# Kernel tuning notes

Hardware: AMD Instinct MI355X
Metric: run time of the kernel (lower is better)

Reference implementation:

```python
import jax, jax.numpy as jnp
import numpy as np

BN_EPS = 1e-5


def _conv1x1(x, w, b=None):
    # x: [B,C,H,W], w: [O,C] (1x1 conv kernel squeezed)
    y = jnp.einsum('bchw,oc->bohw', x, w)
    if b is not None:
        y = y + b[None, :, None, None]
    return y


def _maxpool2(x):
    B, C, H, W = x.shape
    return x.reshape(B, C, H // 2, 2, W // 2, 2).max(axis=(3, 5))


def setup_inputs() -> dict:
    key = jax.random.key(0)
    ks = jax.random.split(key, 14)
    B, C, H, W = 8, 128, 64, 64
    IC = C // 2  # inter_channels
    s = 0.05
    f32 = jnp.float32
    return {
        'x': jax.random.normal(ks[0], (B, C, H, W), f32),
        'w1': jax.random.normal(ks[1], (IC, C), f32) * s,
        'b1': jax.random.normal(ks[2], (IC,), f32) * s,
        'w3': jax.random.normal(ks[3], (IC, C), f32) * s,
        'b3': jax.random.normal(ks[4], (IC,), f32) * s,
        'w4': jax.random.normal(ks[5], (IC, C), f32) * s,
        'b4': jax.random.normal(ks[6], (IC,), f32) * s,
        'w5': jax.random.normal(ks[7], (2 * IC,), f32) * s,  # conv5_pr, no bias
        'w2': jax.random.normal(ks[8], (C, IC), f32) * s,  # zero-init in torch; randomized for a non-trivial baseline
        'b2': jax.random.normal(ks[9], (C,), f32) * s,
        'bn_gamma': 1.0 + jax.random.normal(ks[10], (C,), f32) * 0.1,
        'bn_beta': jax.random.normal(ks[11], (C,), f32) * 0.1,
        'bn_mean': jax.random.normal(ks[12], (C,), f32) * 0.1,
        'bn_var': jax.random.uniform(ks[13], (C,), f32, 0.5, 1.5),
    }


def reference(x, w1, b1, w3, b3, w4, b4, w5, w2, b2, bn_gamma, bn_beta, bn_mean, bn_var):
    B, C, H, W = x.shape
    IC = C // 2
    N = H * W            # query positions
    # value branch: conv1 -> maxpool -> [B, M, IC]
    xg = _maxpool2(_conv1x1(x, w1, b1)).reshape(B, IC, -1)  # [B, IC, M]
    M = xg.shape[-1]
    xg = xg.transpose(0, 2, 1)  # [B, M, IC]
    # affinity: relu(w5 . cat(xt_i, xp_j)) is separable -> avoid [B,2IC,N,M] blowup
    xt = _conv1x1(x, w3, b3).reshape(B, IC, N)              # [B, IC, N]
    xp = _maxpool2(_conv1x1(x, w4, b4)).reshape(B, IC, M)   # [B, IC, M]
    wt, wp = w5[:IC], w5[IC:]
    logits = jnp.einsum('c,bcn->bn', wt, xt)[:, :, None] + \
             jnp.einsum('c,bcm->bm', wp, xp)[:, None, :]    # [B, N, M]
    feats = jax.nn.relu(logits) / M
    # aggregate
    y = jnp.einsum('bnm,bmi->bni', feats, xg)               # [B, N, IC]
    y = y.transpose(0, 2, 1).reshape(B, IC, H, W)
    # conv2 + batchnorm (eval mode, running stats)
    y = _conv1x1(y, w2, b2)
    inv = jax.lax.rsqrt(bn_var + BN_EPS)
    y = (y - bn_mean[None, :, None, None]) * (bn_gamma * inv)[None, :, None, None] + bn_beta[None, :, None, None]
    return y + x
```

## Files before the change

### kernel.cpp

```cpp
#include <hip/hip_runtime.h>

typedef unsigned int u32;
typedef unsigned short u16;

#define Cn 128
#define ICn 64
#define Nn 4096
#define Mn 1024

typedef __attribute__((ext_vector_type(8))) short s8v;
typedef __attribute__((ext_vector_type(4))) float f4v;

__device__ __forceinline__ float bf2f(u16 u){ union{u32 i; float f;} v; v.i = ((u32)u) << 16; return v.f; }
__device__ __forceinline__ u16 f2bf(float f){ union{float f; u32 i;} v; v.f = f; u32 r = v.i + 0x7fffu + ((v.i >> 16) & 1u); return (u16)(r >> 16); }
__device__ __forceinline__ u32 pk2(float lo, float hi){ return (u32)f2bf(lo) | ((u32)f2bf(hi) << 16); }

__global__ __launch_bounds__(256) void k_conv(
    const float* __restrict__ x,
    const float* __restrict__ w1, const float* __restrict__ b1,
    const float* __restrict__ w3, const float* __restrict__ b3,
    const float* __restrict__ w4, const float* __restrict__ b4,
    const float* __restrict__ w5, const float* __restrict__ w2,
    float* __restrict__ t_o, float* __restrict__ p_o, float* __restrict__ g_o)
{
    const int tile = blockIdx.x;
    const int r  = tile >> 1;
    const int wb = tile & 1;
    const int b  = blockIdx.y;
    const int tid = threadIdx.x;

    __shared__ __align__(16) u16 smem[32768];
    u16* xsT = smem;
    u16* w1t = smem + 8704;
    u16* w4t = smem + 17408;
    float* ph = (float*)&smem[26112];
    u16* w2t = smem + 8704;
    u16* xgr = smem + 17920;
    float* u3s = (float*)&smem[30464];

    #pragma unroll
    for (int it = 0; it < 4; ++it) {
        int f = tid + 256 * it;
        int cp = f >> 4, rem = f & 15;
        int rl = rem >> 3, wq = rem & 7;
        const float* src = x + ((size_t)(b * Cn + 2 * cp)) * Nn + (2 * r + rl) * 64 + 32 * wb + 4 * wq;
        float4 v0 = *(const float4*)src;
        float4 v1 = *(const float4*)(src + Nn);
        int lp0 = rl * 32 + 4 * wq;
        int cS = (2 * cp) ^ (wq << 3);
        *(u32*)&xsT[(lp0 + 0) * 136 + cS] = pk2(v0.x, v1.x);
        *(u32*)&xsT[(lp0 + 1) * 136 + cS] = pk2(v0.y, v1.y);
        *(u32*)&xsT[(lp0 + 2) * 136 + cS] = pk2(v0.z, v1.z);
        *(u32*)&xsT[(lp0 + 3) * 136 + cS] = pk2(v0.w, v1.w);
    }
    #pragma unroll
    for (int it = 0; it < 4; ++it) {
        int f = tid + 256 * it;
        int ic = f >> 4, cq = f & 15;
        const float4* s1 = (const float4*)&w1[f * 8];
        const float4* s4 = (const float4*)&w4[f * 8];
        float4 a0 = s1[0], a1v = s1[1];
        float4 d0 = s4[0], d1v = s4[1];
        uint4 A, D;
        A.x = pk2(a0.x, a0.y); A.y = pk2(a0.z, a0.w); A.z = pk2(a1v.x, a1v.y); A.w = pk2(a1v.z, a1v.w);
        D.x = pk2(d0.x, d0.y); D.y = pk2(d0.z, d0.w); D.z = pk2(d1v.x, d1v.y); D.w = pk2(d1v.z, d1v.w);
        *(uint4*)&w1t[ic * 136 + 8 * cq] = A;
        *(uint4*)&w4t[ic * 136 + 8 * cq] = D;
    }
    if (tid < 128) {
        float s0 = 0.f, s1 = 0.f;
        #pragma unroll 8
        for (int ic = 0; ic < 64; ic += 2) {
            s0 += w5[ic]     * w3[ic * Cn + tid];
            s1 += w5[ic + 1] * w3[(ic + 1) * Cn + tid];
        }
        u3s[tid] = s0 + s1;
    } else if (tid == 128) {
        float s = 0.f;
        #pragma unroll 16
        for (int ic = 0; ic < 64; ++ic) s += w5[ic] * b3[ic];
        u3s[128] = s;
    }
    __syncthreads();

    const int lane = tid & 63;
    const int wv   = tid >> 6;
    const int col  = lane & 15;
    const int quad = lane >> 4;

    f4v acc1[4] = {}, acc4[4] = {};
    const u16* xrow = &xsT[(16 * wv + col) * 136];
    const int xsw = (((16 * wv + col) >> 2) & 7) << 3;
    #pragma unroll
    for (int kb = 0; kb < 4; ++kb) {
        s8v bx = *(const s8v*)&xrow[(kb * 32 + quad * 8) ^ xsw];
        #pragma unroll
        for (int icb = 0; icb < 4; ++icb) {
            s8v a1 = *(const s8v*)&w1t[(icb * 16 + col) * 136 + kb * 32 + quad * 8];
            s8v a4 = *(const s8v*)&w4t[(icb * 16 + col) * 136 + kb * 32 + quad * 8];
            acc1[icb] = __builtin_amdgcn_mfma_f32_16x16x32_bf16(a1, bx, acc1[icb], 0, 0, 0);
            acc4[icb] = __builtin_amdgcn_mfma_f32_16x16x32_bf16(a4, bx, acc4[icb], 0, 0, 0);
        }
    }
    __syncthreads();

    const int lp = 16 * wv + col;
    const int rl = lp >> 5, wl = lp & 31, pw = wl >> 1;
    const bool wr = (wl & 1) == 0;
    #pragma unroll
    for (int icb = 0; icb < 4; ++icb)
        #pragma unroll
        for (int reg = 0; reg < 4; ++reg) {
            float v = acc1[icb][reg];
            float vm = fmaxf(v, __shfl_xor(v, 1, 64));
            if (wr) ph[(rl * 16 + pw) * 68 + icb * 16 + quad * 4 + reg] = vm;
        }
    __syncthreads();

    #pragma unroll
    for (int it = 0; it < 4; ++it) {
        int e = tid + 256 * it;
        int pwq = e >> 6, ic = e & 63;
        float v = fmaxf(ph[pwq * 68 + ic], ph[(16 + pwq) * 68 + ic]) + b1[ic];
        xgr[pwq * 72 + ic] = f2bf(v);
    }
    {
        int px = tid >> 2, part = tid & 3;
        const int tsw = ((px >> 2) & 7) << 3;
        const u16* xr = &xsT[px * 136];
        float s = 0.f;
        #pragma unroll
        for (int cq = 0; cq < 4; ++cq) {
            int u = part * 32 + cq * 8;
            s8v xv = *(const s8v*)&xr[u ^ tsw];
            #pragma unroll
            for (int j = 0; j < 8; ++j) s += u3s[u + j] * bf2f((u16)xv[j]);
        }
        s += __shfl_xor(s, 1, 64);
        s += __shfl_xor(s, 2, 64);
        if (part == 0)
            t_o[(size_t)b * Nn + (2 * r + (px >> 5)) * 64 + 32 * wb + (px & 31)] = s + u3s[128];
    }
    __syncthreads();

    #pragma unroll
    for (int it = 0; it < 4; ++it) {
        int f = tid + 256 * it;
        int co = f >> 3, iq = f & 7;
        const float4* s2 = (const float4*)&w2[f * 8];
        float4 a0 = s2[0], a1v = s2[1];
        uint4 V;
        V.x = pk2(a0.x, a0.y); V.y = pk2(a0.z, a0.w); V.z = pk2(a1v.x, a1v.y); V.w = pk2(a1v.z, a1v.w);
        *(uint4*)&w2t[co * 72 + 8 * iq] = V;
    }
    #pragma unroll
    for (int icb = 0; icb < 4; ++icb)
        #pragma unroll
        for (int reg = 0; reg < 4; ++reg) {
            float v = acc4[icb][reg];
            float vm = fmaxf(v, __shfl_xor(v, 1, 64));
            if (wr) ph[(rl * 16 + pw) * 68 + icb * 16 + quad * 4 + reg] = vm;
        }
    __syncthreads();

    #pragma unroll
    for (int cob2 = 0; cob2 < 2; ++cob2) {
        int cob = 2 * wv + cob2;
        f4v gacc = {};
        #pragma unroll
        for (int kb = 0; kb < 2; ++kb) {
            s8v a  = *(const s8v*)&xgr[col * 72 + kb * 32 + quad * 8];
            s8v bb = *(const s8v*)&w2t[(cob * 16 + col) * 72 + kb * 32 + quad * 8];
            gacc = __builtin_amdgcn_mfma_f32_16x16x32_bf16(a, bb, gacc, 0, 0, 0);
        }
        #pragma unroll
        for (int reg = 0; reg < 4; ++reg) {
            int pwr = quad * 4 + reg;
            int m = r * 32 + wb * 16 + pwr;
            g_o[((size_t)b * Mn + m) * 128 + cob * 16 + col] = gacc[reg];
        }
    }

    if (tid < 16) {
        float s = 0.f;
        #pragma unroll 8
        for (int ic = 0; ic < 64; ++ic) {
            float pv = fmaxf(ph[tid * 68 + ic], ph[(16 + tid) * 68 + ic]) + b4[ic];
            s += w5[64 + ic] * pv;
        }
        p_o[(size_t)b * Mn + r * 32 + wb * 16 + tid] = s;
    }
}

__global__ __launch_bounds__(512) void k_rank(
    const float* __restrict__ p, float* __restrict__ ps, int* __restrict__ perm)
{
    const int seg = blockIdx.x;
    const int b   = blockIdx.y;
    const int tid = threadIdx.x;
    __shared__ float pls[1024];
    #pragma unroll
    for (int it = 0; it < 2; ++it) pls[tid + 512 * it] = p[b * 1024 + tid + 512 * it];
    __syncthreads();
    const int m = seg * 32 + (tid >> 4);
    const int sub = tid & 15;
    const float key = pls[m];
    int rank = 0;
    #pragma unroll 8
    for (int jj = 0; jj < 64; ++jj) {
        int j = sub + jj * 16;
        float v = pls[j];
        rank += (v < key || (v == key && j < m)) ? 1 : 0;
    }
    rank += __shfl_xor(rank, 1, 64);
    rank += __shfl_xor(rank, 2, 64);
    rank += __shfl_xor(rank, 4, 64);
    rank += __shfl_xor(rank, 8, 64);
    if (sub == 0) {
        ps[b * 1024 + rank]   = key;
        perm[b * 1024 + rank] = m;
    }
}

__global__ __launch_bounds__(512) void k_scanA(
    const float* __restrict__ g, const float* __restrict__ ps, const int* __restrict__ perm,
    float2* __restrict__ csab)
{
    const int seg = blockIdx.x;
    const int b = blockIdx.y;
    const int tid = threadIdx.x;
    const int co = tid & 127, jh = tid >> 7;
    __shared__ float redA[4][128], redB[4][128];
    __shared__ float pl[32];
    __shared__ int   pml[32];
    if (tid < 32) { pl[tid] = ps[b * 1024 + seg * 32 + tid]; pml[tid] = perm[b * 1024 + seg * 32 + tid]; }
    __syncthreads();
    float sA = 0.f, sB = 0.f;
    #pragma unroll
    for (int jj = jh * 8; jj < jh * 8 + 8; ++jj) {
        float gv = g[((size_t)b * Mn + pml[jj]) * 128 + co];
        sA += gv; sB += pl[jj] * gv;
    }
    redA[jh][co] = sA; redB[jh][co] = sB;
    __syncthreads();
    if (tid < 128) {
        float2 v;
        v.x = (redA[0][tid] + redA[1][tid]) + (redA[2][tid] + redA[3][tid]);
        v.y = (redB[0][tid] + redB[1][tid]) + (redB[2][tid] + redB[3][tid]);
        csab[(b * 32 + seg) * 128 + tid] = v;
    }
}

__global__ __launch_bounds__(512) void k_scanC(
    const float* __restrict__ g, const float* __restrict__ ps, const int* __restrict__ perm,
    const float2* __restrict__ csab, float2* __restrict__ SAB)
{
    const int seg = blockIdx.x;
    const int b = blockIdx.y;
    const int tid = threadIdx.x;
    __shared__ float gs[32 * 128];
    __shared__ float pl[32];
    __shared__ int   pml[32];
    if (tid < 32) { pl[tid] = ps[b * 1024 + seg * 32 + tid]; pml[tid] = perm[b * 1024 + seg * 32 + tid]; }
    __syncthreads();
    #pragma unroll
    for (int it = 0; it < 8; ++it) {
        int f = tid + 512 * it;
        int jj = f >> 7, co = f & 127;
        gs[jj * 128 + co] = g[((size_t)b * Mn + pml[jj]) * 128 + co];
    }
    __syncthreads();

    if (tid < 128) {
        const int co = tid;
        float rA = 0.f, rB = 0.f;
        #pragma unroll 4
        for (int s2 = seg + 1; s2 < 32; ++s2) {
            float2 v = csab[(b * 32 + s2) * 128 + co];
            rA += v.x; rB += v.y;
        }
        if (seg == 31) SAB[((size_t)b * 1025 + 1024) * 128 + co] = make_float2(0.f, 0.f);
        #pragma unroll
        for (int jj = 31; jj >= 0; --jj) {
            float gv = gs[jj * 128 + co];
            rA += gv;
            rB += pl[jj] * gv;
            SAB[((size_t)b * 1025 + seg * 32 + jj) * 128 + co] = make_float2(rA, rB);
        }
    }
}

__global__ __launch_bounds__(512) void k_final(
    const float* __restrict__ x, const float* __restrict__ t,
    const float* __restrict__ ps, const float2* __restrict__ SAB,
    const float* __restrict__ b2, const float* __restrict__ gamma, const float* __restrict__ beta,
    const float* __restrict__ mean, const float* __restrict__ var,
    float* __restrict__ out)
{
    const int nt = blockIdx.x;
    const int b = blockIdx.y;
    const int tid = threadIdx.x;
    const int n0 = nt * 128;
    __shared__ float psl[1024];
    __shared__ float tl[128];
    __shared__ int   kl[128];
    __shared__ float sc[128], bs[128];
    __shared__ float sa_s[32][129], sb_s[32][129];

    #pragma unroll
    for (int it = 0; it < 2; ++it) psl[tid + 512 * it] = ps[b * 1024 + tid + 512 * it];
    __syncthreads();
    if (tid < 128) {
        float tv = t[(size_t)b * Nn + n0 + tid];
        tl[tid] = tv;
        float key = -tv;
        int lo = 0, hi = 1024;
        while (lo < hi) { int mid = (lo + hi) >> 1; if (psl[mid] > key) hi = mid; else lo = mid + 1; }
        kl[tid] = lo;
    } else if (tid < 256) {
        int co = tid - 128;
        float s = gamma[co] * rsqrtf(var[co] + 1e-5f);
        sc[co] = s * (1.0f / 1024.0f);
        bs[co] = (b2[co] - mean[co]) * s + beta[co];
    }
    __syncthreads();

    float2 pf[8], pf2[8];
    {
        #pragma unroll
        for (int i2 = 0; i2 < 8; ++i2) {
            int f = tid + 512 * i2;
            int rowl = f >> 7, co = f & 127;
            pf[i2] = SAB[((size_t)b * 1025 + kl[rowl]) * 128 + co];
        }
    }
    for (int sub = 0; sub < 4; ++sub) {
        #pragma unroll
        for (int i2 = 0; i2 < 8; ++i2) {
            int f = tid + 512 * i2;
            int rowl = f >> 7, co = f & 127;
            sa_s[rowl][co] = pf[i2].x;
            sb_s[rowl][co] = pf[i2].y;
        }
        if (sub < 3) {
            #pragma unroll
            for (int i2 = 0; i2 < 8; ++i2) {
                int f = tid + 512 * i2;
                int rowl = f >> 7, co = f & 127;
                pf2[i2] = SAB[((size_t)b * 1025 + kl[(sub + 1) * 32 + rowl]) * 128 + co];
            }
        }
        __syncthreads();
        #pragma unroll
        for (int it = 0; it < 2; ++it) {
            int f = tid + 512 * it;
            int co = f >> 3, nn0 = (f & 7) * 4;
            size_t gidx = ((size_t)b * Cn + co) * Nn + n0 + sub * 32 + nn0;
            float4 xv = *(const float4*)&x[gidx];
            float scv = sc[co], bsv = bs[co];
            float4 o;
            float v0 = tl[sub*32+nn0+0] * sa_s[nn0+0][co] + sb_s[nn0+0][co];
            float v1 = tl[sub*32+nn0+1] * sa_s[nn0+1][co] + sb_s[nn0+1][co];
            float v2 = tl[sub*32+nn0+2] * sa_s[nn0+2][co] + sb_s[nn0+2][co];
            float v3 = tl[sub*32+nn0+3] * sa_s[nn0+3][co] + sb_s[nn0+3][co];
            o.x = v0 * scv + bsv + xv.x;
            o.y = v1 * scv + bsv + xv.y;
            o.z = v2 * scv + bsv + xv.z;
            o.w = v3 * scv + bsv + xv.w;
            *(float4*)&out[gidx] = o;
        }
        __syncthreads();
        #pragma unroll
        for (int i2 = 0; i2 < 8; ++i2) pf[i2] = pf2[i2];
    }
}

extern "C" void kernel_launch(void* const* d_in, const int* in_sizes, int n_in,
                              void* d_out, int out_size, void* d_ws, size_t ws_size,
                              hipStream_t stream)
{
    const float* x  = (const float*)d_in[0];
    const float* w1 = (const float*)d_in[1];
    const float* b1 = (const float*)d_in[2];
    const float* w3 = (const float*)d_in[3];
    const float* b3 = (const float*)d_in[4];
    const float* w4 = (const float*)d_in[5];
    const float* b4 = (const float*)d_in[6];
    const float* w5 = (const float*)d_in[7];
    const float* w2 = (const float*)d_in[8];
    const float* b2 = (const float*)d_in[9];
    const float* gm = (const float*)d_in[10];
    const float* bt = (const float*)d_in[11];
    const float* mn = (const float*)d_in[12];
    const float* vr = (const float*)d_in[13];
    float* out = (float*)d_out;

    float* ws = (float*)d_ws;
    const size_t FTOT = 3823872;
    if (ws_size < FTOT * sizeof(float)) return;

    float*  t_w  = ws;
    float*  p_w  = ws + 32768;
    float*  ps_w = ws + 40960;
    int*    pm_w = (int*)(ws + 49152);
    float*  g_w  = ws + 581632;
    float2* csab = (float2*)(ws + 1630208);
    float2* SAB  = (float2*)(ws + 1695744);

    k_conv <<<dim3(64, 8), 256, 0, stream>>>(x, w1, b1, w3, b3, w4, b4, w5, w2,
                                             t_w, p_w, g_w);
    k_rank <<<dim3(32, 8), 512, 0, stream>>>(p_w, ps_w, pm_w);
    k_scanA<<<dim3(32, 8), 512, 0, stream>>>(g_w, ps_w, pm_w, csab);
    k_scanC<<<dim3(32, 8), 512, 0, stream>>>(g_w, ps_w, pm_w, csab, SAB);
    k_final<<<dim3(32, 8), 512, 0, stream>>>(x, t_w, ps_w, SAB, b2, gm, bt, mn, vr, out);
}
```

Baseline: 122.5 us.

## Stage conv weights in K-halves, add occupancy bound, and parallelize suffix scan

k_conv now loads the w1/w4 weights into shared memory in two K-halves, each with a 72-element row stride, and adds a launch-bounds min-blocks hint of 3. The shared buffer is re-laid out with byte offsets to fit the new staging plan. k_scanC now uses all 512 threads instead of 128: each group of 128 threads computes a local sum over 8 of the 32 rows, the groups exchange those partial sums through shared memory, and each group then runs its own segment of the reverse scan. The intent is higher occupancy and more parallel work in the scan, at the cost of extra barriers and a second weight-load phase in the conv kernel.

```diff
diff --git a/kernel.cpp b/kernel.cpp
--- a/kernel.cpp
+++ b/kernel.cpp
@@ -15,7 +15,7 @@
 __device__ __forceinline__ u16 f2bf(float f){ union{float f; u32 i;} v; v.f = f; u32 r = v.i + 0x7fffu + ((v.i >> 16) & 1u); return (u16)(r >> 16); }
 __device__ __forceinline__ u32 pk2(float lo, float hi){ return (u32)f2bf(lo) | ((u32)f2bf(hi) << 16); }
 
-__global__ __launch_bounds__(256) void k_conv(
+__global__ __launch_bounds__(256, 3) void k_conv(
     const float* __restrict__ x,
     const float* __restrict__ w1, const float* __restrict__ b1,
     const float* __restrict__ w3, const float* __restrict__ b3,
@@ -29,14 +29,14 @@
     const int b  = blockIdx.y;
     const int tid = threadIdx.x;
 
-    __shared__ __align__(16) u16 smem[32768];
-    u16* xsT = smem;
-    u16* w1t = smem + 8704;
-    u16* w4t = smem + 17408;
-    float* ph = (float*)&smem[26112];
-    u16* w2t = smem + 8704;
-    u16* xgr = smem + 17920;
-    float* u3s = (float*)&smem[30464];
+    __shared__ __align__(16) char smem[47368];
+    u16* xsT = (u16*)smem;
+    u16* wt1 = (u16*)(smem + 17408);
+    u16* wt4 = (u16*)(smem + 26624);
+    u16* w2t = (u16*)(smem + 17408);
+    float* ph = (float*)(smem + 35840);
+    u16* xgr = (u16*)(smem + 44544);
+    float* u3s = (float*)(smem + 46848);
 
     #pragma unroll
     for (int it = 0; it < 4; ++it) {
@@ -54,18 +54,18 @@
         *(u32*)&xsT[(lp0 + 3) * 136 + cS] = pk2(v0.w, v1.w);
     }
     #pragma unroll
-    for (int it = 0; it < 4; ++it) {
+    for (int it = 0; it < 2; ++it) {
         int f = tid + 256 * it;
-        int ic = f >> 4, cq = f & 15;
-        const float4* s1 = (const float4*)&w1[f * 8];
-        const float4* s4 = (const float4*)&w4[f * 8];
-        float4 a0 = s1[0], a1v = s1[1];
-        float4 d0 = s4[0], d1v = s4[1];
+        int ic = f >> 3, cq = f & 7;
+        const float* s1 = &w1[ic * Cn + 8 * cq];
+        const float* s4 = &w4[ic * Cn + 8 * cq];
+        float4 a0 = *(const float4*)s1, a1v = *(const float4*)(s1 + 4);
+        float4 d0 = *(const float4*)s4, d1v = *(const float4*)(s4 + 4);
         uint4 A, D;
         A.x = pk2(a0.x, a0.y); A.y = pk2(a0.z, a0.w); A.z = pk2(a1v.x, a1v.y); A.w = pk2(a1v.z, a1v.w);
         D.x = pk2(d0.x, d0.y); D.y = pk2(d0.z, d0.w); D.z = pk2(d1v.x, d1v.y); D.w = pk2(d1v.z, d1v.w);
-        *(uint4*)&w1t[ic * 136 + 8 * cq] = A;
-        *(uint4*)&w4t[ic * 136 + 8 * cq] = D;
+        *(uint4*)&wt1[ic * 72 + 8 * cq] = A;
+        *(uint4*)&wt4[ic * 72 + 8 * cq] = D;
     }
     if (tid < 128) {
         float s0 = 0.f, s1 = 0.f;
@@ -91,15 +91,38 @@
     f4v acc1[4] = {}, acc4[4] = {};
     const u16* xrow = &xsT[(16 * wv + col) * 136];
     const int xsw = (((16 * wv + col) >> 2) & 7) << 3;
-    #pragma unroll
-    for (int kb = 0; kb < 4; ++kb) {
-        s8v bx = *(const s8v*)&xrow[(kb * 32 + quad * 8) ^ xsw];
-        #pragma unroll
-        for (int icb = 0; icb < 4; ++icb) {
-            s8v a1 = *(const s8v*)&w1t[(icb * 16 + col) * 136 + kb * 32 + quad * 8];
-            s8v a4 = *(const s8v*)&w4t[(icb * 16 + col) * 136 + kb * 32 + quad * 8];
-            acc1[icb] = __builtin_amdgcn_mfma_f32_16x16x32_bf16(a1, bx, acc1[icb], 0, 0, 0);
-            acc4[icb] = __builtin_amdgcn_mfma_f32_16x16x32_bf16(a4, bx, acc4[icb], 0, 0, 0);
+
+    #pragma unroll
+    for (int kh = 0; kh < 2; ++kh) {
+        if (kh == 1) {
+            __syncthreads();
+            #pragma unroll
+            for (int it = 0; it < 2; ++it) {
+                int f = tid + 256 * it;
+                int ic = f >> 3, cq = f & 7;
+                const float* s1 = &w1[ic * Cn + 64 + 8 * cq];
+                const float* s4 = &w4[ic * Cn + 64 + 8 * cq];
+                float4 a0 = *(const float4*)s1, a1v = *(const float4*)(s1 + 4);
+                float4 d0 = *(const float4*)s4, d1v = *(const float4*)(s4 + 4);
+                uint4 A, D;
+                A.x = pk2(a0.x, a0.y); A.y = pk2(a0.z, a0.w); A.z = pk2(a1v.x, a1v.y); A.w = pk2(a1v.z, a1v.w);
+                D.x = pk2(d0.x, d0.y); D.y = pk2(d0.z, d0.w); D.z = pk2(d1v.x, d1v.y); D.w = pk2(d1v.z, d1v.w);
+                *(uint4*)&wt1[ic * 72 + 8 * cq] = A;
+                *(uint4*)&wt4[ic * 72 + 8 * cq] = D;
+            }
+            __syncthreads();
+        }
+        #pragma unroll
+        for (int kb2 = 0; kb2 < 2; ++kb2) {
+            int kb = 2 * kh + kb2;
+            s8v bx = *(const s8v*)&xrow[(kb * 32 + quad * 8) ^ xsw];
+            #pragma unroll
+            for (int icb = 0; icb < 4; ++icb) {
+                s8v a1 = *(const s8v*)&wt1[(icb * 16 + col) * 72 + kb2 * 32 + quad * 8];
+                s8v a4 = *(const s8v*)&wt4[(icb * 16 + col) * 72 + kb2 * 32 + quad * 8];
+                acc1[icb] = __builtin_amdgcn_mfma_f32_16x16x32_bf16(a1, bx, acc1[icb], 0, 0, 0);
+                acc4[icb] = __builtin_amdgcn_mfma_f32_16x16x32_bf16(a4, bx, acc4[icb], 0, 0, 0);
+            }
         }
     }
     __syncthreads();
@@ -261,6 +284,7 @@
     __shared__ float gs[32 * 128];
     __shared__ float pl[32];
     __shared__ int   pml[32];
+    __shared__ float redA[4][128], redB[4][128];
     if (tid < 32) { pl[tid] = ps[b * 1024 + seg * 32 + tid]; pml[tid] = perm[b * 1024 + seg * 32 + tid]; }
     __syncthreads();
     #pragma unroll
@@ -271,22 +295,34 @@
     }
     __syncthreads();
 
-    if (tid < 128) {
-        const int co = tid;
-        float rA = 0.f, rB = 0.f;
-        #pragma unroll 4
-        for (int s2 = seg + 1; s2 < 32; ++s2) {
-            float2 v = csab[(b * 32 + s2) * 128 + co];
-            rA += v.x; rB += v.y;
-        }
-        if (seg == 31) SAB[((size_t)b * 1025 + 1024) * 128 + co] = make_float2(0.f, 0.f);
-        #pragma unroll
-        for (int jj = 31; jj >= 0; --jj) {
-            float gv = gs[jj * 128 + co];
-            rA += gv;
-            rB += pl[jj] * gv;
-            SAB[((size_t)b * 1025 + seg * 32 + jj) * 128 + co] = make_float2(rA, rB);
-        }
+    const int q = tid >> 7;
+    const int co = tid & 127;
+
+    float sA = 0.f, sB = 0.f;
+    #pragma unroll
+    for (int jj = 8 * q; jj < 8 * q + 8; ++jj) {
+        float gv = gs[jj * 128 + co];
+        sA += gv; sB += pl[jj] * gv;
+    }
+    redA[q][co] = sA; redB[q][co] = sB;
+
+    float rA = 0.f, rB = 0.f;
+    #pragma unroll 4
+    for (int s2 = seg + 1; s2 < 32; ++s2) {
+        float2 v = csab[(b * 32 + s2) * 128 + co];
+        rA += v.x; rB += v.y;
+    }
+    __syncthreads();
+    #pragma unroll
+    for (int q2 = q + 1; q2 < 4; ++q2) { rA += redA[q2][co]; rB += redB[q2][co]; }
+
+    if (seg == 31 && tid < 128) SAB[((size_t)b * 1025 + 1024) * 128 + co] = make_float2(0.f, 0.f);
+    #pragma unroll
+    for (int jj = 8 * q + 7; jj >= 8 * q; --jj) {
+        float gv = gs[jj * 128 + co];
+        rA += gv;
+        rB += pl[jj] * gv;
+        SAB[((size_t)b * 1025 + seg * 32 + jj) * 128 + co] = make_float2(rA, rB);
     }
 }
 
```

Result: no change. 124.2 us (+1.4%).

## Fuse rank sort and two-pass suffix scan into one kernel per channel slice

Applied to the files above, without the earlier changes.

Replaces the separate rank, segment-sum and suffix-scan kernels with a single kernel launched per batch and 32-channel slice. Each block recomputes the full rank sort of the 1024 keys in shared memory, then does the chunked suffix scan locally with a shared-memory cross-group combine. This drops two launches and the global round-trips through perm and csab. In exchange the rank computation runs four times per batch, and the grid shrinks to 32 blocks, which leaves most of the GPU idle.

```diff
diff --git a/kernel.cpp b/kernel.cpp
--- a/kernel.cpp
+++ b/kernel.cpp
@@ -192,101 +192,76 @@
     }
 }
 
-__global__ __launch_bounds__(512) void k_rank(
-    const float* __restrict__ p, float* __restrict__ ps, int* __restrict__ perm)
+__global__ __launch_bounds__(512) void k_scan(
+    const float* __restrict__ p, const float* __restrict__ g,
+    float* __restrict__ ps, float2* __restrict__ SAB)
 {
-    const int seg = blockIdx.x;
+    const int csp = blockIdx.x;
     const int b   = blockIdx.y;
     const int tid = threadIdx.x;
-    __shared__ float pls[1024];
-    #pragma unroll
-    for (int it = 0; it < 2; ++it) pls[tid + 512 * it] = p[b * 1024 + tid + 512 * it];
-    __syncthreads();
-    const int m = seg * 32 + (tid >> 4);
-    const int sub = tid & 15;
-    const float key = pls[m];
-    int rank = 0;
+
+    __shared__ __align__(16) float pls[1024];
+    __shared__ __align__(16) float skey[1024];
+    __shared__ int   sm[1024];
+    __shared__ float pA[16][32], pB[16][32];
+
+    pls[tid]       = p[b * 1024 + tid];
+    pls[tid + 512] = p[b * 1024 + tid + 512];
+    __syncthreads();
+
+    {
+        const int m0 = tid, m1 = tid + 512;
+        const float k0 = pls[m0], k1 = pls[m1];
+        int r0 = 0, r1 = 0;
+        #pragma unroll 4
+        for (int j4 = 0; j4 < 256; ++j4) {
+            float4 v = *(const float4*)&pls[4 * j4];
+            int j = 4 * j4;
+            r0 += (v.x < k0 || (v.x == k0 && (j + 0) < m0)) ? 1 : 0;
+            r0 += (v.y < k0 || (v.y == k0 && (j + 1) < m0)) ? 1 : 0;
+            r0 += (v.z < k0 || (v.z == k0 && (j + 2) < m0)) ? 1 : 0;
+            r0 += (v.w < k0 || (v.w == k0 && (j + 3) < m0)) ? 1 : 0;
+            r1 += (v.x < k1 || (v.x == k1 && (j + 0) < m1)) ? 1 : 0;
+            r1 += (v.y < k1 || (v.y == k1 && (j + 1) < m1)) ? 1 : 0;
+            r1 += (v.z < k1 || (v.z == k1 && (j + 2) < m1)) ? 1 : 0;
+            r1 += (v.w < k1 || (v.w == k1 && (j + 3) < m1)) ? 1 : 0;
+        }
+        skey[r0] = k0; sm[r0] = m0;
+        skey[r1] = k1; sm[r1] = m1;
+        if (csp == 0) {
+            ps[b * 1024 + r0] = k0;
+            ps[b * 1024 + r1] = k1;
+        }
+    }
+    __syncthreads();
+
+    const int co32 = tid & 31;
+    const int grp  = tid >> 5;
+    const int co   = csp * 32 + co32;
+    const float* gb = g + (size_t)b * Mn * 128 + co;
+
+    float sA = 0.f, sB = 0.f;
     #pragma unroll 8
-    for (int jj = 0; jj < 64; ++jj) {
-        int j = sub + jj * 16;
-        float v = pls[j];
-        rank += (v < key || (v == key && j < m)) ? 1 : 0;
-    }
-    rank += __shfl_xor(rank, 1, 64);
-    rank += __shfl_xor(rank, 2, 64);
-    rank += __shfl_xor(rank, 4, 64);
-    rank += __shfl_xor(rank, 8, 64);
-    if (sub == 0) {
-        ps[b * 1024 + rank]   = key;
-        perm[b * 1024 + rank] = m;
-    }
-}
-
-__global__ __launch_bounds__(512) void k_scanA(
-    const float* __restrict__ g, const float* __restrict__ ps, const int* __restrict__ perm,
-    float2* __restrict__ csab)
-{
-    const int seg = blockIdx.x;
-    const int b = blockIdx.y;
-    const int tid = threadIdx.x;
-    const int co = tid & 127, jh = tid >> 7;
-    __shared__ float redA[4][128], redB[4][128];
-    __shared__ float pl[32];
-    __shared__ int   pml[32];
-    if (tid < 32) { pl[tid] = ps[b * 1024 + seg * 32 + tid]; pml[tid] = perm[b * 1024 + seg * 32 + tid]; }
-    __syncthreads();
-    float sA = 0.f, sB = 0.f;
-    #pragma unroll
-    for (int jj = jh * 8; jj < jh * 8 + 8; ++jj) {
-        float gv = g[((size_t)b * Mn + pml[jj]) * 128 + co];
-        sA += gv; sB += pl[jj] * gv;
-    }
-    redA[jh][co] = sA; redB[jh][co] = sB;
-    __syncthreads();
-    if (tid < 128) {
-        float2 v;
-        v.x = (redA[0][tid] + redA[1][tid]) + (redA[2][tid] + redA[3][tid]);
-        v.y = (redB[0][tid] + redB[1][tid]) + (redB[2][tid] + redB[3][tid]);
-        csab[(b * 32 + seg) * 128 + tid] = v;
-    }
-}
-
-__global__ __launch_bounds__(512) void k_scanC(
-    const float* __restrict__ g, const float* __restrict__ ps, const int* __restrict__ perm,
-    const float2* __restrict__ csab, float2* __restrict__ SAB)
-{
-    const int seg = blockIdx.x;
-    const int b = blockIdx.y;
-    const int tid = threadIdx.x;
-    __shared__ float gs[32 * 128];
-    __shared__ float pl[32];
-    __shared__ int   pml[32];
-    if (tid < 32) { pl[tid] = ps[b * 1024 + seg * 32 + tid]; pml[tid] = perm[b * 1024 + seg * 32 + tid]; }
-    __syncthreads();
-    #pragma unroll
-    for (int it = 0; it < 8; ++it) {
-        int f = tid + 512 * it;
-        int jj = f >> 7, co = f & 127;
-        gs[jj * 128 + co] = g[((size_t)b * Mn + pml[jj]) * 128 + co];
-    }
-    __syncthreads();
-
-    if (tid < 128) {
-        const int co = tid;
-        float rA = 0.f, rB = 0.f;
-        #pragma unroll 4
-        for (int s2 = seg + 1; s2 < 32; ++s2) {
-            float2 v = csab[(b * 32 + s2) * 128 + co];
-            rA += v.x; rB += v.y;
-        }
-        if (seg == 31) SAB[((size_t)b * 1025 + 1024) * 128 + co] = make_float2(0.f, 0.f);
-        #pragma unroll
-        for (int jj = 31; jj >= 0; --jj) {
-            float gv = gs[jj * 128 + co];
-            rA += gv;
-            rB += pl[jj] * gv;
-            SAB[((size_t)b * 1025 + seg * 32 + jj) * 128 + co] = make_float2(rA, rB);
-        }
+    for (int j = 64 * grp; j < 64 * grp + 64; ++j) {
+        float gv = gb[sm[j] * 128];
+        sA += gv; sB += skey[j] * gv;
+    }
+    pA[grp][co32] = sA; pB[grp][co32] = sB;
+    __syncthreads();
+
+    float rA = 0.f, rB = 0.f;
+    #pragma unroll
+    for (int g2 = grp + 1; g2 < 16; ++g2) { rA += pA[g2][co32]; rB += pB[g2][co32]; }
+
+    float2* SABb = SAB + (size_t)b * 1025 * 128 + co;
+    if (grp == 0) SABb[1024 * 128] = make_float2(0.f, 0.f);
+
+    #pragma unroll 8
+    for (int j = 64 * grp + 63; j >= 64 * grp; --j) {
+        float gv = gb[sm[j] * 128];
+        rA += gv;
+        rB += skey[j] * gv;
+        SABb[j * 128] = make_float2(rA, rB);
     }
 }
 
@@ -402,15 +377,11 @@
     float*  t_w  = ws;
     float*  p_w  = ws + 32768;
     float*  ps_w = ws + 40960;
-    int*    pm_w = (int*)(ws + 49152);
     float*  g_w  = ws + 581632;
-    float2* csab = (float2*)(ws + 1630208);
     float2* SAB  = (float2*)(ws + 1695744);
 
     k_conv <<<dim3(64, 8), 256, 0, stream>>>(x, w1, b1, w3, b3, w4, b4, w5, w2,
                                              t_w, p_w, g_w);
-    k_rank <<<dim3(32, 8), 512, 0, stream>>>(p_w, ps_w, pm_w);
-    k_scanA<<<dim3(32, 8), 512, 0, stream>>>(g_w, ps_w, pm_w, csab);
-    k_scanC<<<dim3(32, 8), 512, 0, stream>>>(g_w, ps_w, pm_w, csab, SAB);
+    k_scan <<<dim3(4, 8),  512, 0, stream>>>(p_w, g_w, ps_w, SAB);
     k_final<<<dim3(32, 8), 512, 0, stream>>>(x, t_w, ps_w, SAB, b2, gm, bt, mn, vr, out);
 }
```

New measurement: 180.9 us. +47.7%, slower.
